# Kernel optimization log

Measured on AMD Instinct MI355X. Metric: run time of the kernel, lower is better.

Reference implementation:

```python
import jax, jax.numpy as jnp
import numpy as np

CLF_LAMBDA = 1.0
SCENARIO_SCALES = (1.0, 1.2)


def setup_inputs() -> dict:
    key = jax.random.key(0)
    ks = jax.random.split(key, 20)
    B, N, H, NC = 65536, 16, 128, 2
    s_in = 1.0 / np.sqrt(N)
    s_h = 1.0 / np.sqrt(H)
    return {
        "x": jax.random.normal(ks[0], (B, N), jnp.float32),
        "V1_w": jax.random.normal(ks[1], (H, N), jnp.float32) * s_in,
        "V1_b": jax.random.normal(ks[2], (H,), jnp.float32) * 0.1,
        "V2_w": jax.random.normal(ks[3], (H, H), jnp.float32) * s_h,
        "V2_b": jax.random.normal(ks[4], (H,), jnp.float32) * 0.1,
        "K1a_w": jax.random.normal(ks[5], (H, N), jnp.float32) * s_in,
        "K1a_b": jax.random.normal(ks[6], (H,), jnp.float32) * 0.1,
        "K1b_w": jax.random.normal(ks[7], (N, H), jnp.float32) * s_h,
        "K1b_b": jax.random.normal(ks[8], (N,), jnp.float32) * 0.1,
        "K2a_w": jax.random.normal(ks[9], (H, N), jnp.float32) * s_in,
        "K2a_b": jax.random.normal(ks[10], (H,), jnp.float32) * 0.1,
        "K2b_w": jax.random.normal(ks[11], (N, H), jnp.float32) * s_h,
        "K2b_b": jax.random.normal(ks[12], (N,), jnp.float32) * 0.1,
        "A_dyn": jax.random.normal(ks[13], (N, N), jnp.float32) * s_in,
        "B_dyn": jax.random.normal(ks[14], (N, NC), jnp.float32) * s_in,
        "x_goal": jax.random.normal(ks[15], (N,), jnp.float32),
        "u_eq": jax.random.normal(ks[16], (NC, 1), jnp.float32),
    }


def _forward(x, V1_w, V1_b, V2_w, V2_b, K1a_w, K1a_b, K1b_w, K1b_b,
             K2a_w, K2a_b, K2b_w, K2b_b, A_dyn, B_dyn, x_goal, u_eq):
    # --- Lyapunov value + manual Jacobian (diag_embed(1-t^2)@W == row-scaling) ---
    t1 = jnp.tanh(x @ V1_w.T + V1_b)                       # [B,H]
    t2 = jnp.tanh(t1 @ V2_w.T + V2_b)                      # [B,H]
    V = 0.5 * jnp.sum(t2 * t2, axis=1)                     # [B]
    D1 = (1.0 - t1 * t1)[:, :, None] * V1_w                # [B,H,N]
    # (diag(1-t2^2) @ V2_w) @ D1, contracted without materializing [B,H,H]
    D2 = jnp.einsum('bh,hk,bkn->bhn', 1.0 - t2 * t2, V2_w, D1)  # [B,H,N]
    grad_V = jnp.einsum('bh,bhn->bn', t2, D2)[:, None, :]  # [B,1,N]

    # --- learned gains K = stack(K1,K2); u = -K (x - x_goal) + u_eq ---
    K1 = jnp.tanh(x @ K1a_w.T + K1a_b) @ K1b_w.T + K1b_b   # [B,N]
    K2 = jnp.tanh(x @ K2a_w.T + K2a_b) @ K2b_w.T + K2b_b   # [B,N]
    K = jnp.stack((K1, K2), axis=1)                        # [B,2,N]
    dx = x - x_goal                                        # [B,N]
    u = -jnp.einsum('bcn,bn->bc', K, dx)[:, :, None] + u_eq  # [B,2,1]

    # --- CLF decrease condition per scenario (linear control-affine dynamics) ---
    gV = grad_V[:, 0, :]                                   # [B,N]
    L_g_V = gV @ B_dyn                                     # [B,NC] (g is state-indep)
    Vdot = jnp.zeros((x.shape[0], 1, 1), x.dtype)
    for scale in SCENARIO_SCALES:
        f = scale * (x @ A_dyn.T)                          # [B,N]
        L_f_V = jnp.sum(gV * f, axis=1)[:, None, None]     # [B,1,1]
        LgVu = jnp.einsum('bc,bco->bo', L_g_V, u)[:, :, None]  # [B,1,1]
        Vdot = Vdot + jax.nn.relu(L_f_V + LgVu + CLF_LAMBDA * V[:, None, None])
    Vdot = Vdot / len(SCENARIO_SCALES)
    relaxation = jnp.zeros((1,), x.dtype)
    return u, relaxation, V, Vdot


def reference(x, V1_w, V1_b, V2_w, V2_b, K1a_w, K1a_b, K1b_w, K1b_b,
              K2a_w, K2a_b, K2b_w, K2b_b, A_dyn, B_dyn, x_goal, u_eq):
    return _forward(x, V1_w, V1_b, V2_w, V2_b, K1a_w, K1a_b, K1b_w, K1b_b,
                    K2a_w, K2a_b, K2b_w, K2b_b, A_dyn, B_dyn, x_goal, u_eq)
```

## Files before the change

### kernel.cpp

```cpp
#include <hip/hip_runtime.h>


typedef __attribute__((ext_vector_type(8))) short bf8_t;
typedef __attribute__((ext_vector_type(4))) float f4_t;
typedef __attribute__((ext_vector_type(4))) short s4_t;

#define MFMA16(a, b, c) __builtin_amdgcn_mfma_f32_16x16x32_bf16((a), (b), (c), 0, 0, 0)

__device__ __forceinline__ float fast_tanh(float v) {
    float e = __builtin_amdgcn_exp2f(v * 2.885390081777927f);
    return 1.0f - 2.0f * __builtin_amdgcn_rcpf(e + 1.0f);
}
__device__ __forceinline__ unsigned short bf16_of(float f) {
    union { float f; unsigned u; } v; v.f = f;
    return (unsigned short)((v.u + 0x8000u) >> 16);
}
__device__ __forceinline__ unsigned pk2(float a, float b) {
    union { float f; unsigned u; } va, vb; va.f = a; vb.f = b;
    return ((va.u + 0x8000u) >> 16) | ((vb.u + 0x8000u) & 0xFFFF0000u);
}
__device__ __forceinline__ float unbf(unsigned short s) {
    union { unsigned u; float f; } v; v.u = ((unsigned)s) << 16; return v.f;
}

__global__ void prep_weights(const float* __restrict__ V1_w,
                             const float* __restrict__ V2_w,
                             const float* __restrict__ K1a_w,
                             const float* __restrict__ K1b_w,
                             const float* __restrict__ K2a_w,
                             const float* __restrict__ K2b_w,
                             const float* __restrict__ A_dyn,
                             unsigned short* __restrict__ ws) {
    int i = blockIdx.x * 256 + threadIdx.x;
    if (i < 2048) {
        ws[i] = bf16_of(V1_w[i]);
        int k = i & 127;
        ws[2048 + i] = bf16_of(V1_w[k * 16 + (i >> 7)]);
        ws[36864 + i] = bf16_of(K1a_w[i]);
        ws[38912 + i] = bf16_of(K2a_w[i]);
        ws[40960 + i] = bf16_of(K1b_w[i]);
        ws[43008 + i] = bf16_of(K2b_w[i]);
    }
    if (i < 16384) {
        ws[4096 + i] = bf16_of(V2_w[i]);
        int k = i >> 7, h = i & 127;
        ws[20480 + i] = bf16_of(V2_w[h * 128 + k]);
    }
    if (i < 256) ws[45056 + i] = bf16_of(A_dyn[i]);
}

__device__ __forceinline__ bf8_t pack8(f4_t a, f4_t b) {
    union { bf8_t v; unsigned u[4]; } r;
    r.u[0] = pk2(a[0], a[1]); r.u[1] = pk2(a[2], a[3]);
    r.u[2] = pk2(b[0], b[1]); r.u[3] = pk2(b[2], b[3]);
    return r.v;
}

__global__ void __launch_bounds__(512) clf_mfma_kernel(
    const float* __restrict__ x,
    const float* __restrict__ V1_b, const float* __restrict__ V2_b,
    const float* __restrict__ K1a_b, const float* __restrict__ K1b_b,
    const float* __restrict__ K2a_b, const float* __restrict__ K2b_b,
    const float* __restrict__ B_dyn, const float* __restrict__ x_goal,
    const float* __restrict__ u_eq,
    const unsigned short* __restrict__ ws, float* __restrict__ out, int B) {
    extern __shared__ unsigned short sm[];
    unsigned short* V2s = sm;
    unsigned short* V2Ts = sm + 16384;
    const int lane = threadIdx.x & 63;
    const int wv = threadIdx.x >> 6;
    const int lr = lane & 15;
    const int g = lane >> 4;
    const int bb = (blockIdx.x * 8 + wv) * 16 + lr;
    unsigned short* bufA = sm + 32768 + wv * 4096;
    unsigned short* bufB = bufA + 2048;

    if (blockIdx.x == 0 && threadIdx.x == 0) out[2 * B] = 0.0f;

#pragma unroll
    for (int q = 0; q < 4; ++q) {
        int e = (q * 512 + threadIdx.x) * 8;
        int r = e >> 7;
        int d = e ^ ((r & 7) << 3);
        *reinterpret_cast<uint4*>(&V2s[d])  = *reinterpret_cast<const uint4*>(ws + 4096 + e);
        *reinterpret_cast<uint4*>(&V2Ts[d]) = *reinterpret_cast<const uint4*>(ws + 20480 + e);
    }
    __syncthreads();

    const unsigned short* wsV1 = ws;
    const unsigned short* wsV1T = ws + 2048;
    const unsigned short* wsK1a = ws + 36864;
    const unsigned short* wsK2a = ws + 38912;
    const unsigned short* wsK1b = ws + 40960;
    const unsigned short* wsK2b = ws + 43008;
    const unsigned short* wsA = ws + 45056;

    const int swz = (lr & 7) << 3;
    auto stA = [&](unsigned short* buf, int h0, unsigned lo, unsigned hi) {
        int idx = (lr * 128 + h0) ^ swz;
        uint2 v; v.x = lo; v.y = hi;
        *reinterpret_cast<uint2*>(buf + idx) = v;
    };
    auto ld8 = [&](const unsigned short* buf, int h0) -> bf8_t {
        int idx = (lr * 128 + h0) ^ swz;
        return *reinterpret_cast<const bf8_t*>(buf + idx);
    };
    auto ld4 = [&](const unsigned short* buf, int h0) -> s4_t {
        int idx = (lr * 128 + h0) ^ swz;
        return *reinterpret_cast<const s4_t*>(buf + idx);
    };
    auto ldW = [&](const unsigned short* Wt, int t, int c) -> bf8_t {
        int idx = ((t * 16 + lr) * 128 + c * 32 + g * 8) ^ swz;
        return *reinterpret_cast<const bf8_t*>(Wt + idx);
    };

    bf8_t xf = {0, 0, 0, 0, 0, 0, 0, 0};
    if (g < 2) {
        const float* xp = x + bb * 16 + g * 8;
        f4_t a = *reinterpret_cast<const f4_t*>(xp);
        f4_t b = *reinterpret_cast<const f4_t*>(xp + 4);
        xf = pack8(a, b);
    }

    auto actnet_lds = [&](const unsigned short* wsW, const float* bias, unsigned short* dst) {
#pragma unroll
        for (int t = 0; t < 8; ++t) {
            bf8_t af = {0, 0, 0, 0, 0, 0, 0, 0};
            if (g < 2) af = *reinterpret_cast<const bf8_t*>(wsW + (t * 16 + lr) * 16 + g * 8);
            f4_t acc = {0.f, 0.f, 0.f, 0.f};
            acc = MFMA16(af, xf, acc);
            f4_t bs = *reinterpret_cast<const f4_t*>(bias + t * 16 + g * 4);
            float v0 = fast_tanh(acc[0] + bs[0]);
            float v1 = fast_tanh(acc[1] + bs[1]);
            float v2 = fast_tanh(acc[2] + bs[2]);
            float v3 = fast_tanh(acc[3] + bs[3]);
            stA(dst, t * 16 + g * 4, pk2(v0, v1), pk2(v2, v3));
        }
    };
    auto actnet_reg = [&](const unsigned short* wsW, const float* bias, unsigned (&W)[8][2]) {
#pragma unroll
        for (int t = 0; t < 8; ++t) {
            bf8_t af = {0, 0, 0, 0, 0, 0, 0, 0};
            if (g < 2) af = *reinterpret_cast<const bf8_t*>(wsW + (t * 16 + lr) * 16 + g * 8);
            f4_t acc = {0.f, 0.f, 0.f, 0.f};
            acc = MFMA16(af, xf, acc);
            f4_t bs = *reinterpret_cast<const f4_t*>(bias + t * 16 + g * 4);
            float v0 = fast_tanh(acc[0] + bs[0]);
            float v1 = fast_tanh(acc[1] + bs[1]);
            float v2 = fast_tanh(acc[2] + bs[2]);
            float v3 = fast_tanh(acc[3] + bs[3]);
            W[t][0] = pk2(v0, v1);
            W[t][1] = pk2(v2, v3);
        }
    };
    auto ksecond = [&](const unsigned short* wsKb, unsigned (&W)[8][2]) -> f4_t {
        f4_t k = {0.f, 0.f, 0.f, 0.f};
        const int srcA = (g & 1) * 32 + lr;
        const int srcB = srcA + 16;
        const bool hi = (g >> 1) != 0;
#pragma unroll
        for (int c = 0; c < 4; ++c) {
            unsigned a0 = __shfl(W[2 * c][0], srcA), b0 = __shfl(W[2 * c + 1][0], srcA);
            unsigned a1 = __shfl(W[2 * c][1], srcA), b1 = __shfl(W[2 * c + 1][1], srcA);
            unsigned a2 = __shfl(W[2 * c][0], srcB), b2 = __shfl(W[2 * c + 1][0], srcB);
            unsigned a3 = __shfl(W[2 * c][1], srcB), b3 = __shfl(W[2 * c + 1][1], srcB);
            union { bf8_t v; unsigned u[4]; } fr;
            fr.u[0] = hi ? b0 : a0;
            fr.u[1] = hi ? b1 : a1;
            fr.u[2] = hi ? b2 : a2;
            fr.u[3] = hi ? b3 : a3;
            const bf8_t* ar = reinterpret_cast<const bf8_t*>(wsKb + lr * 128 + c * 32 + g * 8);
            k = MFMA16(*ar, fr.v, k);
        }
        return k;
    };

    actnet_lds(wsV1, V1_b, bufA);

    unsigned W1r[8][2];
    actnet_reg(wsK1a, K1a_b, W1r);
    f4_t k1 = ksecond(wsK1b, W1r);
    unsigned W2r[8][2];
    actnet_reg(wsK2a, K2a_b, W2r);
    f4_t k2 = ksecond(wsK2b, W2r);

    bf8_t t1f0 = ld8(bufA, 0 + g * 8), t1f1 = ld8(bufA, 32 + g * 8);
    bf8_t t1f2 = ld8(bufA, 64 + g * 8), t1f3 = ld8(bufA, 96 + g * 8);
    float vsum = 0.f;
#pragma unroll
    for (int t = 0; t < 8; ++t) {
        f4_t acc = {0.f, 0.f, 0.f, 0.f};
        acc = MFMA16(ldW(V2s, t, 0), t1f0, acc);
        acc = MFMA16(ldW(V2s, t, 1), t1f1, acc);
        acc = MFMA16(ldW(V2s, t, 2), t1f2, acc);
        acc = MFMA16(ldW(V2s, t, 3), t1f3, acc);
        f4_t bs = *reinterpret_cast<const f4_t*>(V2_b + t * 16 + g * 4);
        float s0, s1, s2v, s3;
        {
            float t2;
            t2 = fast_tanh(acc[0] + bs[0]); vsum = fmaf(t2, t2, vsum); s0 = t2 * (1.f - t2 * t2);
            t2 = fast_tanh(acc[1] + bs[1]); vsum = fmaf(t2, t2, vsum); s1 = t2 * (1.f - t2 * t2);
            t2 = fast_tanh(acc[2] + bs[2]); vsum = fmaf(t2, t2, vsum); s2v = t2 * (1.f - t2 * t2);
            t2 = fast_tanh(acc[3] + bs[3]); vsum = fmaf(t2, t2, vsum); s3 = t2 * (1.f - t2 * t2);
        }
        stA(bufB, t * 16 + g * 4, pk2(s0, s1), pk2(s2v, s3));
    }

    bf8_t s2f0 = ld8(bufB, 0 + g * 8), s2f1 = ld8(bufB, 32 + g * 8);
    bf8_t s2f2 = ld8(bufB, 64 + g * 8), s2f3 = ld8(bufB, 96 + g * 8);
    f4_t wacc[8];
#pragma unroll
    for (int t = 0; t < 8; ++t) {
        f4_t acc = {0.f, 0.f, 0.f, 0.f};
        acc = MFMA16(ldW(V2Ts, t, 0), s2f0, acc);
        acc = MFMA16(ldW(V2Ts, t, 1), s2f1, acc);
        acc = MFMA16(ldW(V2Ts, t, 2), s2f2, acc);
        acc = MFMA16(ldW(V2Ts, t, 3), s2f3, acc);
        wacc[t] = acc;
    }
#pragma unroll
    for (int t = 0; t < 8; ++t) {
        s4_t tv = ld4(bufA, t * 16 + g * 4);
        float c0, c1, c2, c3;
        {
            float t1v;
            t1v = unbf((unsigned short)tv[0]); c0 = wacc[t][0] * (1.f - t1v * t1v);
            t1v = unbf((unsigned short)tv[1]); c1 = wacc[t][1] * (1.f - t1v * t1v);
            t1v = unbf((unsigned short)tv[2]); c2 = wacc[t][2] * (1.f - t1v * t1v);
            t1v = unbf((unsigned short)tv[3]); c3 = wacc[t][3] * (1.f - t1v * t1v);
        }
        stA(bufB, t * 16 + g * 4, pk2(c0, c1), pk2(c2, c3));
    }

    f4_t gacc = {0.f, 0.f, 0.f, 0.f};
    {
        const unsigned short* vr = wsV1T + lr * 128 + g * 8;
        gacc = MFMA16(*reinterpret_cast<const bf8_t*>(vr), ld8(bufB, 0 + g * 8), gacc);
        gacc = MFMA16(*reinterpret_cast<const bf8_t*>(vr + 32), ld8(bufB, 32 + g * 8), gacc);
        gacc = MFMA16(*reinterpret_cast<const bf8_t*>(vr + 64), ld8(bufB, 64 + g * 8), gacc);
        gacc = MFMA16(*reinterpret_cast<const bf8_t*>(vr + 96), ld8(bufB, 96 + g * 8), gacc);
    }

    bf8_t afA = {0, 0, 0, 0, 0, 0, 0, 0};
    if (g < 2) afA = *reinterpret_cast<const bf8_t*>(wsA + lr * 16 + g * 8);
    f4_t fz = {0.f, 0.f, 0.f, 0.f};
    f4_t fac = MFMA16(afA, xf, fz);

    f4_t xv = *reinterpret_cast<const f4_t*>(x + bb * 16 + g * 4);
    f4_t xg = *reinterpret_cast<const f4_t*>(x_goal + g * 4);
    f4_t k1b = *reinterpret_cast<const f4_t*>(K1b_b + g * 4);
    f4_t k2b = *reinterpret_cast<const f4_t*>(K2b_b + g * 4);
    f4_t bd0 = *reinterpret_cast<const f4_t*>(B_dyn + g * 8);
    f4_t bd1 = *reinterpret_cast<const f4_t*>(B_dyn + g * 8 + 4);
    float up0 = 0.f, up1 = 0.f, Lf = 0.f;
#pragma unroll
    for (int r = 0; r < 4; ++r) {
        float dx = xv[r] - xg[r];
        up0 = fmaf(k1[r] + k1b[r], dx, up0);
        up1 = fmaf(k2[r] + k2b[r], dx, up1);
        Lf = fmaf(gacc[r], fac[r], Lf);
    }
    float Lg0 = gacc[0] * bd0[0] + gacc[1] * bd0[2] + gacc[2] * bd1[0] + gacc[3] * bd1[2];
    float Lg1 = gacc[0] * bd0[1] + gacc[1] * bd0[3] + gacc[2] * bd1[1] + gacc[3] * bd1[3];
    up0 += __shfl_xor(up0, 16); up0 += __shfl_xor(up0, 32);
    up1 += __shfl_xor(up1, 16); up1 += __shfl_xor(up1, 32);
    Lf += __shfl_xor(Lf, 16); Lf += __shfl_xor(Lf, 32);
    Lg0 += __shfl_xor(Lg0, 16); Lg0 += __shfl_xor(Lg0, 32);
    Lg1 += __shfl_xor(Lg1, 16); Lg1 += __shfl_xor(Lg1, 32);
    vsum += __shfl_xor(vsum, 16); vsum += __shfl_xor(vsum, 32);

    float u0 = u_eq[0] - up0;
    float u1 = u_eq[1] - up1;
    float V = 0.5f * vsum;
    float G = fmaf(Lg0, u0, fmaf(Lg1, u1, V));
    float Vd = 0.5f * (fmaxf(Lf + G, 0.f) + fmaxf(fmaf(1.2f, Lf, G), 0.f));

    if (g == 0) {
        float2 uo; uo.x = u0; uo.y = u1;
        *reinterpret_cast<float2*>(out + 2 * bb) = uo;
    } else if (g == 1) {
        out[2 * B + 1 + bb] = V;
    } else if (g == 2) {
        out[3 * B + 1 + bb] = Vd;
    }
}

extern "C" void kernel_launch(void* const* d_in, const int* in_sizes, int n_in,
                              void* d_out, int out_size, void* d_ws, size_t ws_size,
                              hipStream_t stream) {
    const float* x = (const float*)d_in[0];
    const float* V1_w = (const float*)d_in[1];
    const float* V1_b = (const float*)d_in[2];
    const float* V2_w = (const float*)d_in[3];
    const float* V2_b = (const float*)d_in[4];
    const float* K1a_w = (const float*)d_in[5];
    const float* K1a_b = (const float*)d_in[6];
    const float* K1b_w = (const float*)d_in[7];
    const float* K1b_b = (const float*)d_in[8];
    const float* K2a_w = (const float*)d_in[9];
    const float* K2a_b = (const float*)d_in[10];
    const float* K2b_w = (const float*)d_in[11];
    const float* K2b_b = (const float*)d_in[12];
    const float* A_dyn = (const float*)d_in[13];
    const float* B_dyn = (const float*)d_in[14];
    const float* x_goal = (const float*)d_in[15];
    const float* u_eq = (const float*)d_in[16];
    float* out = (float*)d_out;
    unsigned short* ws = (unsigned short*)d_ws;

    const int B = in_sizes[0] / 16;
    const size_t smem = 131072;
    (void)hipFuncSetAttribute(reinterpret_cast<const void*>(clf_mfma_kernel),
                              hipFuncAttributeMaxDynamicSharedMemorySize, (int)smem);
    prep_weights<<<64, 256, 0, stream>>>(V1_w, V2_w, K1a_w, K1b_w, K2a_w, K2b_w, A_dyn, ws);
    clf_mfma_kernel<<<512, 512, smem, stream>>>(
        x, V1_b, V2_b, K1a_b, K1b_b, K2a_b, K2b_b,
        B_dyn, x_goal, u_eq, ws, out, B);
}
```

Baseline: 39.63 us.

## Keep per-wave activations in registers via shuffles instead of LDS staging buffers

Intermediate activations (t1, s2, and the Jacobian product) are now regrouped into MFMA B-operand layout with cross-lane shuffles rather than staged through per-wave LDS buffers. This drops shared memory from 128 KB to 64 KB (static, V2 and V2ᵀ only) and adds launch_bounds(512,4) so more blocks can be co-resident per CU. The cost is more register pressure, since T1 must stay live across the whole pipeline, plus extra shuffle instructions. The tighter register cap could cause spills.

```diff
diff --git a/kernel.cpp b/kernel.cpp
--- a/kernel.cpp
+++ b/kernel.cpp
@@ -3,7 +3,6 @@
 
 typedef __attribute__((ext_vector_type(8))) short bf8_t;
 typedef __attribute__((ext_vector_type(4))) float f4_t;
-typedef __attribute__((ext_vector_type(4))) short s4_t;
 
 #define MFMA16(a, b, c) __builtin_amdgcn_mfma_f32_16x16x32_bf16((a), (b), (c), 0, 0, 0)
 
@@ -19,8 +18,11 @@
     union { float f; unsigned u; } va, vb; va.f = a; vb.f = b;
     return ((va.u + 0x8000u) >> 16) | ((vb.u + 0x8000u) & 0xFFFF0000u);
 }
-__device__ __forceinline__ float unbf(unsigned short s) {
-    union { unsigned u; float f; } v; v.u = ((unsigned)s) << 16; return v.f;
+__device__ __forceinline__ float unbf(unsigned s) {
+    union { unsigned u; float f; } v; v.u = s << 16; return v.f;
+}
+__device__ __forceinline__ float unbf_hi(unsigned s) {
+    union { unsigned u; float f; } v; v.u = s & 0xFFFF0000u; return v.f;
 }
 
 __global__ void prep_weights(const float* __restrict__ V1_w,
@@ -56,7 +58,27 @@
     return r.v;
 }
 
-__global__ void __launch_bounds__(512) clf_mfma_kernel(
+__device__ __forceinline__ void regroupB(const unsigned (&W)[8][2], bf8_t (&f)[4],
+                                         int g, int lr) {
+    const int srcA = (g & 1) * 32 + lr;
+    const int srcB = srcA + 16;
+    const bool hi = (g >> 1) != 0;
+#pragma unroll
+    for (int c = 0; c < 4; ++c) {
+        unsigned a0 = __shfl(W[2 * c][0], srcA), b0 = __shfl(W[2 * c + 1][0], srcA);
+        unsigned a1 = __shfl(W[2 * c][1], srcA), b1 = __shfl(W[2 * c + 1][1], srcA);
+        unsigned a2 = __shfl(W[2 * c][0], srcB), b2 = __shfl(W[2 * c + 1][0], srcB);
+        unsigned a3 = __shfl(W[2 * c][1], srcB), b3 = __shfl(W[2 * c + 1][1], srcB);
+        union { bf8_t v; unsigned u[4]; } fr;
+        fr.u[0] = hi ? b0 : a0;
+        fr.u[1] = hi ? b1 : a1;
+        fr.u[2] = hi ? b2 : a2;
+        fr.u[3] = hi ? b3 : a3;
+        f[c] = fr.v;
+    }
+}
+
+__global__ void __launch_bounds__(512, 4) clf_mfma_kernel(
     const float* __restrict__ x,
     const float* __restrict__ V1_b, const float* __restrict__ V2_b,
     const float* __restrict__ K1a_b, const float* __restrict__ K1b_b,
@@ -64,16 +86,13 @@
     const float* __restrict__ B_dyn, const float* __restrict__ x_goal,
     const float* __restrict__ u_eq,
     const unsigned short* __restrict__ ws, float* __restrict__ out, int B) {
-    extern __shared__ unsigned short sm[];
-    unsigned short* V2s = sm;
-    unsigned short* V2Ts = sm + 16384;
+    __shared__ unsigned short V2s[16384];
+    __shared__ unsigned short V2Ts[16384];
     const int lane = threadIdx.x & 63;
     const int wv = threadIdx.x >> 6;
     const int lr = lane & 15;
     const int g = lane >> 4;
     const int bb = (blockIdx.x * 8 + wv) * 16 + lr;
-    unsigned short* bufA = sm + 32768 + wv * 4096;
-    unsigned short* bufB = bufA + 2048;
 
     if (blockIdx.x == 0 && threadIdx.x == 0) out[2 * B] = 0.0f;
 
@@ -96,19 +115,6 @@
     const unsigned short* wsA = ws + 45056;
 
     const int swz = (lr & 7) << 3;
-    auto stA = [&](unsigned short* buf, int h0, unsigned lo, unsigned hi) {
-        int idx = (lr * 128 + h0) ^ swz;
-        uint2 v; v.x = lo; v.y = hi;
-        *reinterpret_cast<uint2*>(buf + idx) = v;
-    };
-    auto ld8 = [&](const unsigned short* buf, int h0) -> bf8_t {
-        int idx = (lr * 128 + h0) ^ swz;
-        return *reinterpret_cast<const bf8_t*>(buf + idx);
-    };
-    auto ld4 = [&](const unsigned short* buf, int h0) -> s4_t {
-        int idx = (lr * 128 + h0) ^ swz;
-        return *reinterpret_cast<const s4_t*>(buf + idx);
-    };
     auto ldW = [&](const unsigned short* Wt, int t, int c) -> bf8_t {
         int idx = ((t * 16 + lr) * 128 + c * 32 + g * 8) ^ swz;
         return *reinterpret_cast<const bf8_t*>(Wt + idx);
@@ -122,21 +128,6 @@
         xf = pack8(a, b);
     }
 
-    auto actnet_lds = [&](const unsigned short* wsW, const float* bias, unsigned short* dst) {
-#pragma unroll
-        for (int t = 0; t < 8; ++t) {
-            bf8_t af = {0, 0, 0, 0, 0, 0, 0, 0};
-            if (g < 2) af = *reinterpret_cast<const bf8_t*>(wsW + (t * 16 + lr) * 16 + g * 8);
-            f4_t acc = {0.f, 0.f, 0.f, 0.f};
-            acc = MFMA16(af, xf, acc);
-            f4_t bs = *reinterpret_cast<const f4_t*>(bias + t * 16 + g * 4);
-            float v0 = fast_tanh(acc[0] + bs[0]);
-            float v1 = fast_tanh(acc[1] + bs[1]);
-            float v2 = fast_tanh(acc[2] + bs[2]);
-            float v3 = fast_tanh(acc[3] + bs[3]);
-            stA(dst, t * 16 + g * 4, pk2(v0, v1), pk2(v2, v3));
-        }
-    };
     auto actnet_reg = [&](const unsigned short* wsW, const float* bias, unsigned (&W)[8][2]) {
 #pragma unroll
         for (int t = 0; t < 8; ++t) {
@@ -153,47 +144,41 @@
             W[t][1] = pk2(v2, v3);
         }
     };
-    auto ksecond = [&](const unsigned short* wsKb, unsigned (&W)[8][2]) -> f4_t {
+    auto kmul = [&](const unsigned short* wsKb, const bf8_t (&f)[4]) -> f4_t {
         f4_t k = {0.f, 0.f, 0.f, 0.f};
-        const int srcA = (g & 1) * 32 + lr;
-        const int srcB = srcA + 16;
-        const bool hi = (g >> 1) != 0;
 #pragma unroll
         for (int c = 0; c < 4; ++c) {
-            unsigned a0 = __shfl(W[2 * c][0], srcA), b0 = __shfl(W[2 * c + 1][0], srcA);
-            unsigned a1 = __shfl(W[2 * c][1], srcA), b1 = __shfl(W[2 * c + 1][1], srcA);
-            unsigned a2 = __shfl(W[2 * c][0], srcB), b2 = __shfl(W[2 * c + 1][0], srcB);
-            unsigned a3 = __shfl(W[2 * c][1], srcB), b3 = __shfl(W[2 * c + 1][1], srcB);
-            union { bf8_t v; unsigned u[4]; } fr;
-            fr.u[0] = hi ? b0 : a0;
-            fr.u[1] = hi ? b1 : a1;
-            fr.u[2] = hi ? b2 : a2;
-            fr.u[3] = hi ? b3 : a3;
             const bf8_t* ar = reinterpret_cast<const bf8_t*>(wsKb + lr * 128 + c * 32 + g * 8);
-            k = MFMA16(*ar, fr.v, k);
+            k = MFMA16(*ar, f[c], k);
         }
         return k;
     };
 
-    actnet_lds(wsV1, V1_b, bufA);
+    unsigned T1[8][2];
+    actnet_reg(wsV1, V1_b, T1);
+    bf8_t t1f[4];
+    regroupB(T1, t1f, g, lr);
 
     unsigned W1r[8][2];
     actnet_reg(wsK1a, K1a_b, W1r);
-    f4_t k1 = ksecond(wsK1b, W1r);
+    bf8_t a1f[4];
+    regroupB(W1r, a1f, g, lr);
+    f4_t k1 = kmul(wsK1b, a1f);
     unsigned W2r[8][2];
     actnet_reg(wsK2a, K2a_b, W2r);
-    f4_t k2 = ksecond(wsK2b, W2r);
-
-    bf8_t t1f0 = ld8(bufA, 0 + g * 8), t1f1 = ld8(bufA, 32 + g * 8);
-    bf8_t t1f2 = ld8(bufA, 64 + g * 8), t1f3 = ld8(bufA, 96 + g * 8);
+    bf8_t a2f[4];
+    regroupB(W2r, a2f, g, lr);
+    f4_t k2 = kmul(wsK2b, a2f);
+
+    unsigned S2[8][2];
     float vsum = 0.f;
 #pragma unroll
     for (int t = 0; t < 8; ++t) {
         f4_t acc = {0.f, 0.f, 0.f, 0.f};
-        acc = MFMA16(ldW(V2s, t, 0), t1f0, acc);
-        acc = MFMA16(ldW(V2s, t, 1), t1f1, acc);
-        acc = MFMA16(ldW(V2s, t, 2), t1f2, acc);
-        acc = MFMA16(ldW(V2s, t, 3), t1f3, acc);
+        acc = MFMA16(ldW(V2s, t, 0), t1f[0], acc);
+        acc = MFMA16(ldW(V2s, t, 1), t1f[1], acc);
+        acc = MFMA16(ldW(V2s, t, 2), t1f[2], acc);
+        acc = MFMA16(ldW(V2s, t, 3), t1f[3], acc);
         f4_t bs = *reinterpret_cast<const f4_t*>(V2_b + t * 16 + g * 4);
         float s0, s1, s2v, s3;
         {
@@ -203,43 +188,39 @@
             t2 = fast_tanh(acc[2] + bs[2]); vsum = fmaf(t2, t2, vsum); s2v = t2 * (1.f - t2 * t2);
             t2 = fast_tanh(acc[3] + bs[3]); vsum = fmaf(t2, t2, vsum); s3 = t2 * (1.f - t2 * t2);
         }
-        stA(bufB, t * 16 + g * 4, pk2(s0, s1), pk2(s2v, s3));
-    }
-
-    bf8_t s2f0 = ld8(bufB, 0 + g * 8), s2f1 = ld8(bufB, 32 + g * 8);
-    bf8_t s2f2 = ld8(bufB, 64 + g * 8), s2f3 = ld8(bufB, 96 + g * 8);
+        S2[t][0] = pk2(s0, s1);
+        S2[t][1] = pk2(s2v, s3);
+    }
+    bf8_t s2f[4];
+    regroupB(S2, s2f, g, lr);
+
     f4_t wacc[8];
 #pragma unroll
     for (int t = 0; t < 8; ++t) {
         f4_t acc = {0.f, 0.f, 0.f, 0.f};
-        acc = MFMA16(ldW(V2Ts, t, 0), s2f0, acc);
-        acc = MFMA16(ldW(V2Ts, t, 1), s2f1, acc);
-        acc = MFMA16(ldW(V2Ts, t, 2), s2f2, acc);
-        acc = MFMA16(ldW(V2Ts, t, 3), s2f3, acc);
+        acc = MFMA16(ldW(V2Ts, t, 0), s2f[0], acc);
+        acc = MFMA16(ldW(V2Ts, t, 1), s2f[1], acc);
+        acc = MFMA16(ldW(V2Ts, t, 2), s2f[2], acc);
+        acc = MFMA16(ldW(V2Ts, t, 3), s2f[3], acc);
         wacc[t] = acc;
     }
+
+    unsigned C[8][2];
 #pragma unroll
     for (int t = 0; t < 8; ++t) {
-        s4_t tv = ld4(bufA, t * 16 + g * 4);
-        float c0, c1, c2, c3;
-        {
-            float t1v;
-            t1v = unbf((unsigned short)tv[0]); c0 = wacc[t][0] * (1.f - t1v * t1v);
-            t1v = unbf((unsigned short)tv[1]); c1 = wacc[t][1] * (1.f - t1v * t1v);
-            t1v = unbf((unsigned short)tv[2]); c2 = wacc[t][2] * (1.f - t1v * t1v);
-            t1v = unbf((unsigned short)tv[3]); c3 = wacc[t][3] * (1.f - t1v * t1v);
-        }
-        stA(bufB, t * 16 + g * 4, pk2(c0, c1), pk2(c2, c3));
-    }
-
-    f4_t gacc = {0.f, 0.f, 0.f, 0.f};
-    {
-        const unsigned short* vr = wsV1T + lr * 128 + g * 8;
-        gacc = MFMA16(*reinterpret_cast<const bf8_t*>(vr), ld8(bufB, 0 + g * 8), gacc);
-        gacc = MFMA16(*reinterpret_cast<const bf8_t*>(vr + 32), ld8(bufB, 32 + g * 8), gacc);
-        gacc = MFMA16(*reinterpret_cast<const bf8_t*>(vr + 64), ld8(bufB, 64 + g * 8), gacc);
-        gacc = MFMA16(*reinterpret_cast<const bf8_t*>(vr + 96), ld8(bufB, 96 + g * 8), gacc);
-    }
+        float t0v = unbf(T1[t][0]), t1v = unbf_hi(T1[t][0]);
+        float t2v = unbf(T1[t][1]), t3v = unbf_hi(T1[t][1]);
+        float c0 = wacc[t][0] * (1.f - t0v * t0v);
+        float c1 = wacc[t][1] * (1.f - t1v * t1v);
+        float c2 = wacc[t][2] * (1.f - t2v * t2v);
+        float c3 = wacc[t][3] * (1.f - t3v * t3v);
+        C[t][0] = pk2(c0, c1);
+        C[t][1] = pk2(c2, c3);
+    }
+    bf8_t cf[4];
+    regroupB(C, cf, g, lr);
+
+    f4_t gacc = kmul(wsV1T, cf);
 
     bf8_t afA = {0, 0, 0, 0, 0, 0, 0, 0};
     if (g < 2) afA = *reinterpret_cast<const bf8_t*>(wsA + lr * 16 + g * 8);
@@ -309,11 +290,8 @@
     unsigned short* ws = (unsigned short*)d_ws;
 
     const int B = in_sizes[0] / 16;
-    const size_t smem = 131072;
-    (void)hipFuncSetAttribute(reinterpret_cast<const void*>(clf_mfma_kernel),
-                              hipFuncAttributeMaxDynamicSharedMemorySize, (int)smem);
     prep_weights<<<64, 256, 0, stream>>>(V1_w, V2_w, K1a_w, K1b_w, K2a_w, K2b_w, A_dyn, ws);
-    clf_mfma_kernel<<<512, 512, smem, stream>>>(
+    clf_mfma_kernel<<<512, 512, 0, stream>>>(
         x, V1_b, V2_b, K1a_b, K1b_b, K2a_b, K2b_b,
         B_dyn, x_goal, u_eq, ws, out, B);
 }
```

New measurement: 53.09 us. 34.0% more time.
